# Kernel tuning notes

Measured on AMD Instinct MI355X. Metric: run time of the kernel, lower is better.

Reference implementation:

```python
import jax, jax.numpy as jnp
import numpy as np

B, C, H, W = 8, 128, 64, 64

def setup_inputs() -> dict:
    key = jax.random.key(0)
    ks = jax.random.split(key, 7)
    s = 1.0 / np.sqrt(C)
    return {
        "x": jax.random.normal(ks[0], (B, C, H, W), dtype=jnp.float32),
        "Wq": jax.random.normal(ks[1], (C, C), dtype=jnp.float32) * s,
        "bq": jax.random.normal(ks[2], (C,), dtype=jnp.float32) * 0.01,
        "Wk": jax.random.normal(ks[3], (C, C), dtype=jnp.float32) * s,
        "bk": jax.random.normal(ks[4], (C,), dtype=jnp.float32) * 0.01,
        "Wv": jax.random.normal(ks[5], (C, C), dtype=jnp.float32) * s,
        "bv": jax.random.normal(ks[6], (C,), dtype=jnp.float32) * 0.01,
    }

def reference(x, Wq, bq, Wk, bk, Wv, bv):
    b, c, h, w = x.shape
    n = h * w
    scale = 1.0 / jnp.sqrt(jnp.asarray(c, x.dtype))
    xf = x.reshape(b, c, n)                                   # [B,C,N]
    # 1x1 convs == per-pixel linear layers
    q = jnp.einsum('oc,bcn->bno', Wq, xf) + bq                # [B,N,C]
    k = jnp.einsum('oc,bcn->bcn', Wk, xf) + bk[None, :, None] # [B,C,N]
    v = jnp.einsum('oc,bcn->bno', Wv, xf) + bv                # [B,N,C]
    attn = jax.nn.softmax(jnp.einsum('bnc,bcm->bnm', q, k) * scale, axis=-1)
    out = jnp.einsum('bnm,bmc->bnc', attn, v)                 # [B,N,C]
    return x + out.transpose(0, 2, 1).reshape(b, c, h, w)
```

## Files before the change

kernel.cpp:

```cpp
#include <hip/hip_runtime.h>

#define BB 8
#define CC 128
#define NN 4096

typedef __bf16 bf16x8_t __attribute__((ext_vector_type(8)));
typedef unsigned short u16x8 __attribute__((ext_vector_type(8)));
typedef float f32x4 __attribute__((ext_vector_type(4)));
typedef unsigned int u32x4 __attribute__((ext_vector_type(4)));
typedef __attribute__((address_space(1))) const unsigned int gu32;
typedef __attribute__((address_space(3))) unsigned int lu32;

#define KSCALE 0.12753262456033348f

__device__ __forceinline__ unsigned short f2bf(float f) {
  unsigned int u = __builtin_bit_cast(unsigned int, f);
  u += 0x7fffu + ((u >> 16) & 1u);
  return (unsigned short)(u >> 16);
}

__device__ __forceinline__ float bf2f(unsigned short s) {
  unsigned int u = ((unsigned int)s) << 16;
  return __builtin_bit_cast(float, u);
}

__device__ __forceinline__ unsigned int cvt_pk_bf16(float lo, float hi) {
  unsigned int r;
  asm("v_cvt_pk_bf16_f32 %0, %1, %2" : "=v"(r) : "v"(lo), "v"(hi));
  return r;
}

__device__ __forceinline__ f32x4 mfma16(u16x8 a, u16x8 b, f32x4 c) {
  return __builtin_amdgcn_mfma_f32_16x16x32_bf16(
      __builtin_bit_cast(bf16x8_t, a), __builtin_bit_cast(bf16x8_t, b), c, 0, 0, 0);
}

__global__ void prep(const float* __restrict__ Wq, const float* __restrict__ Wv,
                     const float* __restrict__ Wk,
                     unsigned short* __restrict__ Qwb, unsigned short* __restrict__ Vwb,
                     float* __restrict__ csk) {
  if (blockIdx.x < 64) {
    const int i = blockIdx.x * 256 + threadIdx.x;
    Qwb[i] = f2bf(Wq[i] * KSCALE);
    Vwb[i] = f2bf(Wv[i]);
  } else if (threadIdx.x < CC) {
    const int c = threadIdx.x;
    float s = 0.f;
    for (int o = 0; o < CC; ++o) s += Wk[(size_t)o * CC + c];
    csk[c] = s;
  }
}

__global__ __launch_bounds__(256, 2) void qkv_proj(
    const float* __restrict__ x,
    const unsigned short* __restrict__ Qwb, const float* __restrict__ bq,
    const float* __restrict__ csk, const float* __restrict__ bk,
    const unsigned short* __restrict__ Vwb, const float* __restrict__ bv,
    unsigned short* __restrict__ Q,
    unsigned short* __restrict__ K,
    unsigned short* __restrict__ V)
{
  const int b  = blockIdx.x & 7;
  const int n0 = (blockIdx.x >> 3) << 6;
  const int t  = threadIdx.x;
  const int lane = t & 63;
  const int w  = t >> 6;
  const int lq = lane & 15;
  const int g  = lane >> 4;

  __shared__ unsigned short xs[64][136];
  __shared__ unsigned short ks[64][136];
  __shared__ unsigned short vs[128][72];

  {
    const int n = t & 63;
    const float* xp = x + (size_t)b * (CC * NN) + n0 + n;
    for (int c = t >> 6; c < CC; c += 4) {
      const float xv = xp[(size_t)c * NN];
      xs[n][c] = f2bf(xv);
      ks[n][c] = f2bf(xv * csk[c] + bk[c]);
    }
  }
  __syncthreads();

  u16x8 a[4];
  {
    const unsigned short* ap = &xs[w * 16 + lq][g * 8];
    for (int ksl = 0; ksl < 4; ++ksl) a[ksl] = *(const u16x8*)(ap + ksl * 32);
  }

  for (int ot = 0; ot < 8; ++ot) {
    f32x4 aq = {0.f,0.f,0.f,0.f}, av = {0.f,0.f,0.f,0.f};
    const int o = ot * 16 + lq;
    const unsigned short* wq = Qwb + (size_t)o * CC + g * 8;
    const unsigned short* wv = Vwb + (size_t)o * CC + g * 8;
    for (int ksl = 0; ksl < 4; ++ksl) {
      aq = mfma16(a[ksl], *(const u16x8*)(wq + ksl * 32), aq);
      av = mfma16(a[ksl], *(const u16x8*)(wv + ksl * 32), av);
    }
    const float bqv = bq[o] * KSCALE, bvv = bv[o];
    for (int r = 0; r < 4; ++r) {
      const int nl = w * 16 + g * 4 + r;
      Q[((size_t)b * NN + n0 + nl) * CC + o] = f2bf(aq[r] + bqv);
      vs[o][nl] = f2bf(av[r] + bvv);
    }
  }
  __syncthreads();

  {
    unsigned short* kout = K + ((size_t)b * NN + n0) * CC;
    for (int i = t; i < 64 * 16; i += 256) {
      const int n = i >> 4, oc = (i & 15) * 8;
      *(uint4*)(kout + (size_t)n * CC + oc) = *(const uint4*)&ks[n][oc];
    }
  }
  {
    unsigned short* vout = V + (size_t)b * (CC * NN) + n0;
    for (int i = t; i < 128 * 32; i += 256) {
      const int c  = i >> 5;
      const int np = (i & 31) << 1;
      *(unsigned int*)(vout + (size_t)c * NN + np) = *(const unsigned int*)&vs[c][np];
    }
  }
}

__global__ __launch_bounds__(512, 4) void flash_attn(
    const unsigned short* __restrict__ Q,
    const unsigned short* __restrict__ K,
    const unsigned short* __restrict__ V,
    unsigned short* __restrict__ PO,
    float2* __restrict__ PML)
{
  const int bid = blockIdx.x;
  const int b  = bid & 7;
  const int qb = (bid >> 3) & 31;
  const int sp = bid >> 8;
  const int kv0 = sp << 11;
  const int t  = threadIdx.x;
  const int lane = t & 63;
  const int w  = t >> 6;
  const int lq = lane & 15;
  const int g  = lane >> 4;
  const int q0w = (qb << 7) + (w << 4);

  __shared__ unsigned short KtL[2][64 * 128];
  __shared__ unsigned short VlL[2][128 * 64];

  u16x8 qf[4];
  {
    const unsigned short* qp = Q + ((size_t)b * NN + q0w + lq) * CC + g * 8;
    #pragma unroll
    for (int ksl = 0; ksl < 4; ++ksl) qf[ksl] = *(const u16x8*)(qp + ksl * 32);
  }

  const char* kgb = (const char*)(K + (size_t)b * NN * CC);
  const char* vgb = (const char*)(V + (size_t)b * CC * NN);
  int soK[2];
  #pragma unroll
  for (int j = 0; j < 2; ++j) {
    const int p = t * 16 + j * 8192;
    const int row = p >> 8;
    soK[j] = (p & ~255) | ((p & 255) ^ ((row & 15) << 4));
  }
  int vOff[8];
  #pragma unroll
  for (int n = 0; n < 8; ++n) {
    const int p = t * 4 + n * 2048;
    const int ch = p >> 7;
    const int L = (p & 127) ^ ((ch & 7) << 4);
    const int gb = (L & 7) | (((L >> 4) & 3) << 3) | (((L >> 3) & 1) << 5) | ((L >> 6) << 6);
    vOff[n] = ch * (NN * 2) + gb;
  }

  #define STAGE(nb, kv) do {                                                      \
    const char* kg_ = kgb + ((size_t)(kv) << 8);                                  \
    const char* vg_ = vgb + ((size_t)(kv) << 1);                                  \
    _Pragma("unroll")                                                             \
    for (int j = 0; j < 2; ++j)                                                   \
      __builtin_amdgcn_global_load_lds((gu32*)(kg_ + soK[j]),                     \
          (lu32*)((char*)KtL + (nb) * 16384 + t * 16 + j * 8192), 16, 0, 0);      \
    _Pragma("unroll")                                                             \
    for (int n = 0; n < 8; ++n)                                                   \
      __builtin_amdgcn_global_load_lds((gu32*)(vg_ + vOff[n]),                    \
          (lu32*)((char*)VlL + (nb) * 16384 + t * 4 + n * 2048), 4, 0, 0);        \
  } while (0)

  f32x4 oacc[8];
  #pragma unroll
  for (int i = 0; i < 8; ++i) oacc[i] = f32x4{0.f, 0.f, 0.f, 0.f};
  float m_run = -1e30f, l_run = 0.f;

  const int swzK  = lq << 4;
  const int swzVl = (lq & 7) << 4;

  STAGE(0, kv0);

  for (int tt = 0; tt < 32; ++tt) {
    const int cur = tt & 1;
    if (tt < 31) {
      STAGE(cur ^ 1, kv0 + (tt + 1) * 64);
      asm volatile("s_waitcnt vmcnt(10)" ::: "memory");
    } else {
      asm volatile("s_waitcnt vmcnt(0)" ::: "memory");
    }
    __builtin_amdgcn_s_barrier();

    const char* kb  = (const char*)KtL + cur * 16384;
    const char* vbb = (const char*)VlL + cur * 16384;

    f32x4 s[4];
    #pragma unroll
    for (int kt = 0; kt < 4; ++kt) s[kt] = f32x4{0.f, 0.f, 0.f, 0.f};
    __builtin_amdgcn_s_setprio(1);
    #pragma unroll
    for (int kt = 0; kt < 4; ++kt) {
      const char* kp = kb + (kt * 16 + lq) * 256;
      #pragma unroll
      for (int ksl = 0; ksl < 4; ++ksl) {
        u16x8 kf = *(const u16x8*)(kp + ((ksl * 64 + g * 16) ^ swzK));
        s[kt] = mfma16(kf, qf[ksl], s[kt]);
      }
    }
    __builtin_amdgcn_s_setprio(0);

    float pa = fmaxf(fmaxf(s[0][0], s[0][1]), s[0][2]);
    float pb = fmaxf(fmaxf(s[0][3], s[1][0]), s[1][1]);
    float pc = fmaxf(fmaxf(s[1][2], s[1][3]), s[2][0]);
    float pd = fmaxf(fmaxf(s[2][1], s[2][2]), s[2][3]);
    float pe = fmaxf(fmaxf(s[3][0], s[3][1]), s[3][2]);
    float pm = fmaxf(fmaxf(pa, pb), pc);
    pm = fmaxf(fmaxf(pm, pd), fmaxf(pe, s[3][3]));
    pm = fmaxf(pm, __shfl_xor(pm, 16));
    pm = fmaxf(pm, __shfl_xor(pm, 32));
    if (!__all(pm - m_run <= 8.0f)) {
      const float m_new = fmaxf(m_run, pm);
      const float alpha = exp2f(m_run - m_new);
      l_run *= alpha;
      #pragma unroll
      for (int i = 0; i < 8; ++i) {
        oacc[i][0] *= alpha; oacc[i][1] *= alpha;
        oacc[i][2] *= alpha; oacc[i][3] *= alpha;
      }
      m_run = m_new;
    }
    float lsum = 0.f;
    unsigned pkw[8];
    #pragma unroll
    for (int kt = 0; kt < 4; ++kt) {
      const float e0 = exp2f(s[kt][0] - m_run), e1 = exp2f(s[kt][1] - m_run);
      const float e2 = exp2f(s[kt][2] - m_run), e3 = exp2f(s[kt][3] - m_run);
      lsum += (e0 + e1) + (e2 + e3);
      pkw[kt * 2 + 0] = cvt_pk_bf16(e0, e1);
      pkw[kt * 2 + 1] = cvt_pk_bf16(e2, e3);
    }
    lsum += __shfl_xor(lsum, 16);
    lsum += __shfl_xor(lsum, 32);
    l_run += lsum;

    u32x4 pw0 = {pkw[0], pkw[1], pkw[2], pkw[3]};
    u32x4 pw1 = {pkw[4], pkw[5], pkw[6], pkw[7]};
    const u16x8 pf0 = __builtin_bit_cast(u16x8, pw0);
    const u16x8 pf1 = __builtin_bit_cast(u16x8, pw1);
    __builtin_amdgcn_s_setprio(1);
    #pragma unroll
    for (int dt = 0; dt < 8; ++dt) {
      const char* vp = vbb + (dt * 16 + lq) * 128;
      u16x8 vf0 = *(const u16x8*)(vp + ((g * 16) ^ swzVl));
      oacc[dt] = mfma16(vf0, pf0, oacc[dt]);
      u16x8 vf1 = *(const u16x8*)(vp + ((64 + g * 16) ^ swzVl));
      oacc[dt] = mfma16(vf1, pf1, oacc[dt]);
    }
    __builtin_amdgcn_s_setprio(0);
    asm volatile("s_waitcnt lgkmcnt(0)" ::: "memory");
    __builtin_amdgcn_s_barrier();
  }
  #undef STAGE

  const float rinv = 1.0f / l_run;
  const int n = q0w + lq;
  unsigned short* po = PO + (size_t)sp * (BB * CC * NN) + (size_t)b * (CC * NN);
  #pragma unroll
  for (int dt = 0; dt < 8; ++dt) {
    #pragma unroll
    for (int r = 0; r < 4; ++r) {
      const int c = dt * 16 + g * 4 + r;
      po[(size_t)c * NN + n] = f2bf(oacc[dt][r] * rinv);
    }
  }
  if (g == 0) PML[((size_t)sp * BB + b) * NN + n] = float2{m_run, l_run};
}

__global__ __launch_bounds__(256) void combine(
    const float* __restrict__ x,
    const unsigned short* __restrict__ PO,
    const float2* __restrict__ PML,
    float* __restrict__ out)
{
  const size_t base = ((size_t)blockIdx.x * 256 + threadIdx.x) * 4;
  const int n = (int)(base & 4095);
  const int b = (int)(base >> 19);
  const float2 ml0 = PML[(size_t)b * NN + n];
  const float2 ml1 = PML[(size_t)(BB + b) * NN + n];
  const float M = fmaxf(ml0.x, ml1.x);
  float w0 = ml0.y * exp2f(ml0.x - M);
  float w1 = ml1.y * exp2f(ml1.x - M);
  const float inv = 1.0f / (w0 + w1);
  w0 *= inv; w1 *= inv;

  ushort4 o0 = *(const ushort4*)(PO + base);
  ushort4 o1 = *(const ushort4*)(PO + (size_t)BB * CC * NN + base);
  float4 xv = *(const float4*)(x + base);
  float4 r;
  r.x = xv.x + w0 * bf2f(o0.x) + w1 * bf2f(o1.x);
  r.y = xv.y + w0 * bf2f(o0.y) + w1 * bf2f(o1.y);
  r.z = xv.z + w0 * bf2f(o0.z) + w1 * bf2f(o1.z);
  r.w = xv.w + w0 * bf2f(o0.w) + w1 * bf2f(o1.w);
  *(float4*)(out + base) = r;
}

extern "C" void kernel_launch(void* const* d_in, const int* in_sizes, int n_in,
                              void* d_out, int out_size, void* d_ws, size_t ws_size,
                              hipStream_t stream) {
  (void)in_sizes; (void)n_in; (void)out_size; (void)ws_size;
  const float* x  = (const float*)d_in[0];
  const float* Wq = (const float*)d_in[1];
  const float* bq = (const float*)d_in[2];
  const float* Wk = (const float*)d_in[3];
  const float* bk = (const float*)d_in[4];
  const float* Wv = (const float*)d_in[5];
  const float* bv = (const float*)d_in[6];

  unsigned short* Q   = (unsigned short*)d_ws;
  unsigned short* K   = Q + (size_t)BB * NN * CC;
  unsigned short* V   = K + (size_t)BB * NN * CC;
  unsigned short* PO  = V + (size_t)BB * NN * CC;
  float2* PML         = (float2*)(PO + (size_t)2 * BB * CC * NN);
  unsigned short* Qwb = (unsigned short*)(PML + (size_t)2 * BB * NN);
  unsigned short* Vwb = Qwb + (size_t)CC * CC;
  float* csk = (float*)(Vwb + (size_t)CC * CC);
  float* out = (float*)d_out;

  prep<<<dim3(65), dim3(256), 0, stream>>>(Wq, Wv, Wk, Qwb, Vwb, csk);
  qkv_proj<<<dim3(BB * (NN / 64)), dim3(256), 0, stream>>>(x, Qwb, bq, csk, bk, Vwb, bv, Q, K, V);
  flash_attn<<<dim3(BB * 32 * 2), dim3(512), 0, stream>>>(Q, K, V, PO, PML);
  combine<<<dim3((BB * CC * NN) / (256 * 4)), dim3(256), 0, stream>>>(x, PO, PML, out);
}
```

Baseline: 139.1 us.

## Defer softmax max rescale by exponentiating with stale max folded into MFMA init

The QK^T accumulators are now initialised to the negated running max, so scores come out already shifted and go straight into exp2 with no separate max pass before the PV matmul. The max check moves after the PV MFMAs and runs on the exponentiated values. When any exponent exceeds 256 (a max jump over 8 in log2 units), the accumulators and the denominator are rescaled by the reciprocal of that exponent. This takes the cross-lane max reduction and the branch off the critical path between the two matmuls, so the exp work can overlap with the MFMAs. In exchange, the bf16 probabilities for that tile can be as large as 2^8 or more before correction, which risks precision or overflow if the first tile's max is far below later ones.

```diff
diff --git a/kernel.cpp b/kernel.cpp
--- a/kernel.cpp
+++ b/kernel.cpp
@@ -188,7 +188,7 @@
   f32x4 oacc[8];
   #pragma unroll
   for (int i = 0; i < 8; ++i) oacc[i] = f32x4{0.f, 0.f, 0.f, 0.f};
-  float m_run = -1e30f, l_run = 0.f;
+  float m_run = 0.f, l_run = 0.f;
 
   const int swzK  = lq << 4;
   const int swzVl = (lq & 7) << 4;
@@ -208,9 +208,10 @@
     const char* kb  = (const char*)KtL + cur * 16384;
     const char* vbb = (const char*)VlL + cur * 16384;
 
+    const float mneg = -m_run;
     f32x4 s[4];
     #pragma unroll
-    for (int kt = 0; kt < 4; ++kt) s[kt] = f32x4{0.f, 0.f, 0.f, 0.f};
+    for (int kt = 0; kt < 4; ++kt) s[kt] = f32x4{mneg, mneg, mneg, mneg};
     __builtin_amdgcn_s_setprio(1);
     #pragma unroll
     for (int kt = 0; kt < 4; ++kt) {
@@ -223,39 +224,27 @@
     }
     __builtin_amdgcn_s_setprio(0);
 
+    #pragma unroll
+    for (int kt = 0; kt < 4; ++kt) {
+      s[kt][0] = exp2f(s[kt][0]); s[kt][1] = exp2f(s[kt][1]);
+      s[kt][2] = exp2f(s[kt][2]); s[kt][3] = exp2f(s[kt][3]);
+    }
+
+    float lsum = 0.f;
+    unsigned pkw[8];
+    #pragma unroll
+    for (int kt = 0; kt < 4; ++kt) {
+      lsum += (s[kt][0] + s[kt][1]) + (s[kt][2] + s[kt][3]);
+      pkw[kt * 2 + 0] = cvt_pk_bf16(s[kt][0], s[kt][1]);
+      pkw[kt * 2 + 1] = cvt_pk_bf16(s[kt][2], s[kt][3]);
+    }
     float pa = fmaxf(fmaxf(s[0][0], s[0][1]), s[0][2]);
     float pb = fmaxf(fmaxf(s[0][3], s[1][0]), s[1][1]);
     float pc = fmaxf(fmaxf(s[1][2], s[1][3]), s[2][0]);
     float pd = fmaxf(fmaxf(s[2][1], s[2][2]), s[2][3]);
     float pe = fmaxf(fmaxf(s[3][0], s[3][1]), s[3][2]);
-    float pm = fmaxf(fmaxf(pa, pb), pc);
-    pm = fmaxf(fmaxf(pm, pd), fmaxf(pe, s[3][3]));
-    pm = fmaxf(pm, __shfl_xor(pm, 16));
-    pm = fmaxf(pm, __shfl_xor(pm, 32));
-    if (!__all(pm - m_run <= 8.0f)) {
-      const float m_new = fmaxf(m_run, pm);
-      const float alpha = exp2f(m_run - m_new);
-      l_run *= alpha;
-      #pragma unroll
-      for (int i = 0; i < 8; ++i) {
-        oacc[i][0] *= alpha; oacc[i][1] *= alpha;
-        oacc[i][2] *= alpha; oacc[i][3] *= alpha;
-      }
-      m_run = m_new;
-    }
-    float lsum = 0.f;
-    unsigned pkw[8];
-    #pragma unroll
-    for (int kt = 0; kt < 4; ++kt) {
-      const float e0 = exp2f(s[kt][0] - m_run), e1 = exp2f(s[kt][1] - m_run);
-      const float e2 = exp2f(s[kt][2] - m_run), e3 = exp2f(s[kt][3] - m_run);
-      lsum += (e0 + e1) + (e2 + e3);
-      pkw[kt * 2 + 0] = cvt_pk_bf16(e0, e1);
-      pkw[kt * 2 + 1] = cvt_pk_bf16(e2, e3);
-    }
-    lsum += __shfl_xor(lsum, 16);
-    lsum += __shfl_xor(lsum, 32);
-    l_run += lsum;
+    float pmE = fmaxf(fmaxf(pa, pb), pc);
+    pmE = fmaxf(fmaxf(pmE, pd), fmaxf(pe, s[3][3]));
 
     u32x4 pw0 = {pkw[0], pkw[1], pkw[2], pkw[3]};
     u32x4 pw1 = {pkw[4], pkw[5], pkw[6], pkw[7]};
@@ -271,6 +260,24 @@
       oacc[dt] = mfma16(vf1, pf1, oacc[dt]);
     }
     __builtin_amdgcn_s_setprio(0);
+
+    pmE  = fmaxf(pmE, __shfl_xor(pmE, 16));
+    pmE  = fmaxf(pmE, __shfl_xor(pmE, 32));
+    lsum += __shfl_xor(lsum, 16);
+    lsum += __shfl_xor(lsum, 32);
+    if (!__all(pmE <= 256.0f)) {
+      const float d = __log2f(pmE);
+      const float alpha = exp2f(-d);
+      m_run += d;
+      l_run = (l_run + lsum) * alpha;
+      #pragma unroll
+      for (int i = 0; i < 8; ++i) {
+        oacc[i][0] *= alpha; oacc[i][1] *= alpha;
+        oacc[i][2] *= alpha; oacc[i][3] *= alpha;
+      }
+    } else {
+      l_run += lsum;
+    }
     asm volatile("s_waitcnt lgkmcnt(0)" ::: "memory");
     __builtin_amdgcn_s_barrier();
   }
```

After: 155.6 us. 11.9% more time.
